# Kernel optimization log

Hardware: AMD Instinct MI355X
Metric: run time of the kernel (lower is better)

The kernel has to match this reference:

```python
import jax, jax.numpy as jnp
import numpy as np

EMBED = 1024
HIDDEN = 4 * EMBED
NUM_EXPERTS = 8
TOP_K = 2


def setup_inputs() -> dict:
    key = jax.random.key(0)
    k_in, k_w1, k_b1, k_w2, k_b2 = jax.random.split(key, 5)
    s1 = 1.0 / np.sqrt(EMBED)
    s2 = 1.0 / np.sqrt(HIDDEN)
    return {
        "inputs": jax.random.normal(k_in, (8, 4096, EMBED), dtype=jnp.float32),
        "w1": jax.random.uniform(k_w1, (EMBED, HIDDEN), jnp.float32, -s1, s1),
        "b1": jax.random.uniform(k_b1, (HIDDEN,), jnp.float32, -s1, s1),
        "w2": jax.random.uniform(k_w2, (HIDDEN, NUM_EXPERTS), jnp.float32, -s2, s2),
        "b2": jax.random.uniform(k_b2, (NUM_EXPERTS,), jnp.float32, -s2, s2),
    }


def reference(inputs, w1, b1, w2, b2):
    # MLP scorer: [B,S,E] -> [B,S,H] -> [B,S,num_experts]
    h = jax.nn.relu(jnp.einsum("bse,eh->bsh", inputs, w1) + b1)
    score = jnp.einsum("bsh,hn->bsn", h, w2) + b2
    # top-k over expert dim
    _, topk_idx = jax.lax.top_k(score, TOP_K)  # [B,S,K]
    # scatter mask: True at top-k positions
    mask = jax.nn.one_hot(topk_idx, NUM_EXPERTS, dtype=jnp.bool_).any(axis=-2)  # [B,S,N]
    masked = jnp.where(mask, score, -jnp.inf)
    router_output = jax.nn.softmax(masked, axis=-1)
    return router_output, topk_idx
```

## Files before the change

### kernel.cpp

```cpp
#include <hip/hip_runtime.h>

#define T_TOK 32768
#define EDIM  1024
#define HDIM  4096
#define NEXP  8
#define TAU   1.0e-3f
#define MAXR  8192


typedef _Float16 f16x8 __attribute__((ext_vector_type(8)));
typedef _Float16 f16x4 __attribute__((ext_vector_type(4)));
typedef __attribute__((ext_vector_type(4))) float f32x4;
#define MFMA16(a, b, c) __builtin_amdgcn_mfma_f32_16x16x32_f16(a, b, c, 0, 0, 0)

__device__ __forceinline__ void gload16(const void* g, void* l) {
    __builtin_amdgcn_global_load_lds(
        (const __attribute__((address_space(1))) void*)g,
        (__attribute__((address_space(3))) void*)l, 16, 0, 0);
}

__global__ __launch_bounds__(256) void split_x_kernel(
    const float* __restrict__ x, _Float16* __restrict__ hi, int n4)
{
    int i = blockIdx.x * 256 + threadIdx.x;
    int stride = gridDim.x * 256;
    for (; i < n4; i += stride) {
        float4 v = ((const float4*)x)[i];
        f16x4 h;
        h[0] = (_Float16)v.x; h[1] = (_Float16)v.y;
        h[2] = (_Float16)v.z; h[3] = (_Float16)v.w;
        *(f16x4*)&hi[i * 4] = h;
    }
}

__global__ __launch_bounds__(256) void split_w1t_kernel(
    const float* __restrict__ w1, _Float16* __restrict__ thi)
{
    __shared__ float t[64][65];
    const int ht = blockIdx.x;
    const int et = blockIdx.y;
    const int tid = threadIdx.x;
    const int er = tid >> 6, hc = tid & 63;
#pragma unroll
    for (int rr = 0; rr < 16; ++rr) {
        int e = rr * 4 + er;
        t[e][hc] = w1[(size_t)(et * 64 + e) * HDIM + ht * 64 + hc];
    }
    __syncthreads();
    const int hl = tid >> 2, eg = tid & 3;
    size_t base = (size_t)(ht * 64 + hl) * EDIM + et * 64 + eg * 16;
#pragma unroll
    for (int q = 0; q < 4; ++q) {
        f16x4 a;
#pragma unroll
        for (int z = 0; z < 4; ++z) a[z] = (_Float16)t[eg * 16 + q * 4 + z][hl];
        *(f16x4*)&thi[base + q * 4] = a;
    }
}

__global__ __launch_bounds__(256, 3) void mfma_score_kernel(
    const _Float16* __restrict__ xhi, const _Float16* __restrict__ whi,
    const float* __restrict__ b1, const float* __restrict__ w2,
    float* __restrict__ part)
{
    __shared__ __align__(16) _Float16 A3[3 * 4096];
    __shared__ __align__(16) _Float16 B3[3 * 4096];

    const int bid = blockIdx.x;
    const int lg  = (bid & 7) * 1024 + (bid >> 3);
    const int ht  = (lg >> 10) * 4 + (lg & 3);
    const int mt  = (lg & 1023) >> 2;
    const int m0 = mt * 128;
    const int h0 = ht * 128;
    const int tid = threadIdx.x;
    const int l = tid & 63;
    const int wid = tid >> 6;
    const int wm = wid >> 1, wn = wid & 1;

    const int srow = tid >> 2;
    const int sg = (tid & 3) ^ ((srow >> 1) & 3);
    const size_t xa0 = (size_t)(m0 + srow) * EDIM + sg * 8;
    const size_t xa1 = (size_t)(m0 + 64 + srow) * EDIM + sg * 8;
    const size_t wa0 = (size_t)(h0 + srow) * EDIM + sg * 8;
    const size_t wa1 = (size_t)(h0 + 64 + srow) * EDIM + sg * 8;
    const int ldst = tid * 16;

    const int lrow = l & 15, lslot = l >> 4;
    const int rslot = lslot ^ ((lrow >> 1) & 3);
    const int aoff = (wm * 64 + lrow) * 64 + rslot * 16;
    const int boff = (wn * 64 + lrow) * 64 + rslot * 16;

    f32x4 accA[4][4];
    const f32x4 zz = {0.f, 0.f, 0.f, 0.f};
#pragma unroll
    for (int i = 0; i < 4; ++i)
#pragma unroll
        for (int j = 0; j < 4; ++j) accA[i][j] = zz;

    auto stage = [&](int s, int bb) {
        const int k0 = s * 32;
        gload16(xhi + xa0 + k0, (char*)A3 + bb * 8192 + ldst);
        gload16(xhi + xa1 + k0, (char*)A3 + bb * 8192 + 4096 + ldst);
        gload16(whi + wa0 + k0, (char*)B3 + bb * 8192 + ldst);
        gload16(whi + wa1 + k0, (char*)B3 + bb * 8192 + 4096 + ldst);
    };
    auto compute = [&](int bb) {
        const char* Ab = (const char*)A3 + bb * 8192;
        const char* Bb = (const char*)B3 + bb * 8192;
        f16x8 ah[4];
#pragma unroll
        for (int mf = 0; mf < 4; ++mf)
            ah[mf] = *(const f16x8*)(Ab + aoff + mf * 1024);
        __builtin_amdgcn_s_setprio(1);
#pragma unroll
        for (int nf = 0; nf < 4; ++nf) {
            f16x8 bh = *(const f16x8*)(Bb + boff + nf * 1024);
#pragma unroll
            for (int mf = 0; mf < 4; ++mf)
                accA[mf][nf] = MFMA16(ah[mf], bh, accA[mf][nf]);
        }
        __builtin_amdgcn_s_setprio(0);
    };

#define WAITV4 do { asm volatile("s_waitcnt vmcnt(4)" ::: "memory"); \
                    __builtin_amdgcn_sched_barrier(0); } while (0)
#define WAITV0 do { asm volatile("s_waitcnt vmcnt(0)" ::: "memory"); \
                    __builtin_amdgcn_sched_barrier(0); } while (0)
#define BARR   do { __builtin_amdgcn_s_barrier(); \
                    __builtin_amdgcn_sched_barrier(0); } while (0)

    stage(0, 0);
    stage(1, 1);

    for (int t = 0; t < 30; t += 3) {
        WAITV4; BARR; stage(t + 2, (t + 2) % 3); compute(0);
        WAITV4; BARR; stage(t + 3, (t + 3) % 3); compute(1);
        WAITV4; BARR; stage(t + 4, (t + 4) % 3); compute(2);
    }
    WAITV4; BARR; compute(0);
    WAITV0; BARR; compute(1);

#undef WAITV4
#undef WAITV0
#undef BARR

    float b1r[4], w2r[4][8];
#pragma unroll
    for (int nf = 0; nf < 4; ++nf) {
        int h = h0 + wn * 64 + nf * 16 + lrow;
        b1r[nf] = b1[h];
#pragma unroll
        for (int n = 0; n < 8; ++n) w2r[nf][n] = w2[(size_t)h * NEXP + n];
    }

    const int b0 = l & 1, b1b = (l >> 1) & 1, b2 = (l >> 2) & 1, b3 = (l >> 3) & 1;
    const int regf = (b0 << 1) | b1b;
    const int n0e  = b2 * 4 + b3 * 2;
    float outq[4][2];

#pragma unroll
    for (int q = 0; q < 4; ++q) {
        float v[32];
#pragma unroll
        for (int i = 0; i < 32; ++i) v[i] = 0.f;
#pragma unroll
        for (int reg = 0; reg < 4; ++reg)
#pragma unroll
            for (int nf = 0; nf < 4; ++nf) {
                float hv = fmaxf(accA[q][nf][reg] + b1r[nf], 0.f);
#pragma unroll
                for (int n = 0; n < 8; ++n)
                    v[reg * 8 + n] = fmaf(hv, w2r[nf][n], v[reg * 8 + n]);
            }
        float t1[16];
#pragma unroll
        for (int i = 0; i < 16; ++i) {
            float keep = b0 ? v[i + 16] : v[i];
            float send = b0 ? v[i] : v[i + 16];
            t1[i] = keep + __shfl_xor(send, 1);
        }
        float t2[8];
#pragma unroll
        for (int i = 0; i < 8; ++i) {
            float keep = b1b ? t1[i + 8] : t1[i];
            float send = b1b ? t1[i] : t1[i + 8];
            t2[i] = keep + __shfl_xor(send, 2);
        }
        float t3[4];
#pragma unroll
        for (int i = 0; i < 4; ++i) {
            float keep = b2 ? t2[i + 4] : t2[i];
            float send = b2 ? t2[i] : t2[i + 4];
            t3[i] = keep + __shfl_xor(send, 4);
        }
#pragma unroll
        for (int j = 0; j < 2; ++j) {
            float keep = b3 ? t3[j + 2] : t3[j];
            float send = b3 ? t3[j] : t3[j + 2];
            outq[q][j] = keep + __shfl_xor(send, 8);
        }
    }

    __syncthreads();
    float* red = (float*)A3;
    if (wn == 1) {
#pragma unroll
        for (int q = 0; q < 4; ++q) {
            red[(wm * 64 + l) * 8 + q * 2 + 0] = outq[q][0];
            red[(wm * 64 + l) * 8 + q * 2 + 1] = outq[q][1];
        }
    }
    __syncthreads();
    if (wn == 0) {
#pragma unroll
        for (int q = 0; q < 4; ++q) {
            float a = outq[q][0] + red[(wm * 64 + l) * 8 + q * 2 + 0];
            float b = outq[q][1] + red[(wm * 64 + l) * 8 + q * 2 + 1];
            int rl = wm * 64 + q * 16 + lslot * 4 + regf;
            *(float2*)&part[((size_t)ht * T_TOK + m0 + rl) * NEXP + n0e] =
                make_float2(a, b);
        }
    }
}

__global__ void zero_counter_kernel(int* c) {
    if (threadIdx.x == 0 && blockIdx.x == 0) *c = 0;
}

__global__ __launch_bounds__(256) void router_finish_kernel(
    const float* __restrict__ part, const float* __restrict__ b2,
    float* __restrict__ out, int nparts, int* __restrict__ counter,
    int* __restrict__ list)
{
    int t = blockIdx.x * 256 + threadIdx.x;
    if (t >= T_TOK) return;

    float s[NEXP];
#pragma unroll
    for (int n = 0; n < NEXP; ++n) s[n] = 0.f;
    for (int p = 0; p < nparts; ++p) {
        const float* ps = part + (size_t)p * T_TOK * NEXP + (size_t)t * NEXP;
        float4 v0 = *reinterpret_cast<const float4*>(ps);
        float4 v1 = *reinterpret_cast<const float4*>(ps + 4);
        s[0] += v0.x; s[1] += v0.y; s[2] += v0.z; s[3] += v0.w;
        s[4] += v1.x; s[5] += v1.y; s[6] += v1.z; s[7] += v1.w;
    }
#pragma unroll
    for (int n = 0; n < NEXP; ++n) s[n] += b2[n];

    int i1 = 0; float v1 = s[0];
#pragma unroll
    for (int n = 1; n < NEXP; ++n) { if (s[n] > v1) { v1 = s[n]; i1 = n; } }
    int i2 = -1; float v2 = -3.402823466e38f;
#pragma unroll
    for (int n = 0; n < NEXP; ++n) { if (n != i1 && s[n] > v2) { v2 = s[n]; i2 = n; } }
    float v3 = -3.402823466e38f;
#pragma unroll
    for (int n = 0; n < NEXP; ++n) { if (n != i1 && n != i2 && s[n] > v3) v3 = s[n]; }

    if ((v1 - v2) < TAU || (v2 - v3) < TAU) {
        int pos = atomicAdd(counter, 1);
        list[pos] = t;
    }

    float e2 = expf(v2 - v1);
    float denom = 1.f + e2;
    float p1 = 1.f / denom;
    float p2 = e2 / denom;
#pragma unroll
    for (int n = 0; n < NEXP; ++n)
        out[(size_t)t * NEXP + n] = (n == i1) ? p1 : ((n == i2) ? p2 : 0.f);
    out[(size_t)T_TOK * NEXP + (size_t)t * 2 + 0] = (float)i1;
    out[(size_t)T_TOK * NEXP + (size_t)t * 2 + 1] = (float)i2;
}

__global__ __launch_bounds__(256) void gather_x_kernel(
    const float* __restrict__ x, const int* __restrict__ counter,
    const int* __restrict__ list, float* __restrict__ xg)
{
    int cnt = *counter; if (cnt > MAXR) cnt = MAXR;
    for (int g = blockIdx.x; g < cnt; g += gridDim.x) {
        const int t = list[g];
        float4 v = ((const float4*)(x + (size_t)t * EDIM))[threadIdx.x];
        ((float4*)(xg + (size_t)g * EDIM))[threadIdx.x] = v;
    }
}

__global__ __launch_bounds__(256) void refine_gemm_kernel(
    const float* __restrict__ xg, const float* __restrict__ w1,
    const float* __restrict__ b1, const float* __restrict__ w2,
    const int* __restrict__ counter, float* __restrict__ rpart)
{
    int cnt = *counter; if (cnt > MAXR) cnt = MAXR;
    const int m0 = blockIdx.y * 64;
    if (m0 >= cnt) return;
    const int ht = blockIdx.x;
    const int h0 = ht * 128;
    const int tid = threadIdx.x;
    const int tx = tid & 15, ty = tid >> 4;

    __shared__ float xs[16][68];
    __shared__ float wsh[16][128];

    float acc[4][8];
#pragma unroll
    for (int i = 0; i < 4; ++i)
#pragma unroll
        for (int j = 0; j < 8; ++j) acc[i][j] = 0.f;

    const int lk = tid & 15, lt = tid >> 4;
    const int lh = tid & 127, lkg = tid >> 7;

    for (int k0 = 0; k0 < EDIM; k0 += 16) {
        __syncthreads();
#pragma unroll
        for (int r = 0; r < 4; ++r)
            xs[lk][lt + r * 16] = xg[(size_t)(m0 + lt + r * 16) * EDIM + k0 + lk];
#pragma unroll
        for (int r = 0; r < 8; ++r)
            wsh[lkg + r * 2][lh] = w1[(size_t)(k0 + lkg + r * 2) * HDIM + h0 + lh];
        __syncthreads();
#pragma unroll
        for (int k = 0; k < 16; ++k) {
            float a[4], b[8];
#pragma unroll
            for (int i = 0; i < 4; ++i) a[i] = xs[k][ty * 4 + i];
            *reinterpret_cast<float4*>(&b[0]) = *reinterpret_cast<const float4*>(&wsh[k][tx * 8]);
            *reinterpret_cast<float4*>(&b[4]) = *reinterpret_cast<const float4*>(&wsh[k][tx * 8 + 4]);
#pragma unroll
            for (int i = 0; i < 4; ++i)
#pragma unroll
                for (int j = 0; j < 8; ++j)
                    acc[i][j] = fmaf(a[i], b[j], acc[i][j]);
        }
    }

    float sred[4][NEXP];
#pragma unroll
    for (int i = 0; i < 4; ++i) {
        float hv[8];
#pragma unroll
        for (int j = 0; j < 8; ++j)
            hv[j] = fmaxf(acc[i][j] + b1[h0 + tx * 8 + j], 0.f);
#pragma unroll
        for (int n = 0; n < NEXP; ++n) {
            float ssum = 0.f;
#pragma unroll
            for (int j = 0; j < 8; ++j)
                ssum = fmaf(hv[j], w2[(size_t)(h0 + tx * 8 + j) * NEXP + n], ssum);
            sred[i][n] = ssum;
        }
    }
#pragma unroll
    for (int i = 0; i < 4; ++i)
#pragma unroll
        for (int n = 0; n < NEXP; ++n) {
            float v = sred[i][n];
            v += __shfl_xor(v, 1);
            v += __shfl_xor(v, 2);
            v += __shfl_xor(v, 4);
            v += __shfl_xor(v, 8);
            sred[i][n] = v;
        }

    if (tx == 0) {
#pragma unroll
        for (int i = 0; i < 4; ++i) {
            int g = m0 + ty * 4 + i;
            if (g < cnt) {
#pragma unroll
                for (int n = 0; n < NEXP; ++n)
                    rpart[((size_t)g * 32 + ht) * NEXP + n] = sred[i][n];
            }
        }
    }
}

__global__ __launch_bounds__(256) void refine_final_kernel(
    const int* __restrict__ counter, const int* __restrict__ list,
    const float* __restrict__ rpart, const float* __restrict__ b2,
    float* __restrict__ out)
{
    int cnt = *counter; if (cnt > MAXR) cnt = MAXR;
    const int g = blockIdx.x * 256 + threadIdx.x;
    if (g >= cnt) return;
    const int t = list[g];
    float s[NEXP];
#pragma unroll
    for (int n = 0; n < NEXP; ++n) s[n] = b2[n];
    for (int r = 0; r < 32; ++r)
#pragma unroll
        for (int n = 0; n < NEXP; ++n)
            s[n] += rpart[((size_t)g * 32 + r) * NEXP + n];

    int i1 = 0; float v1 = s[0];
#pragma unroll
    for (int n = 1; n < NEXP; ++n) { if (s[n] > v1) { v1 = s[n]; i1 = n; } }
    int i2 = -1; float v2 = -3.402823466e38f;
#pragma unroll
    for (int n = 0; n < NEXP; ++n) { if (n != i1 && s[n] > v2) { v2 = s[n]; i2 = n; } }

    float e2 = expf(v2 - v1);
    float denom = 1.f + e2;
    float p1 = 1.f / denom;
    float p2 = e2 / denom;
#pragma unroll
    for (int n = 0; n < NEXP; ++n)
        out[(size_t)t * NEXP + n] = (n == i1) ? p1 : ((n == i2) ? p2 : 0.f);
    out[(size_t)T_TOK * NEXP + (size_t)t * 2 + 0] = (float)i1;
    out[(size_t)T_TOK * NEXP + (size_t)t * 2 + 1] = (float)i2;
}

#define BM 128
#define BH 128
#define BK 16
#define NHT (HDIM / BH)

__global__ __launch_bounds__(256) void score_gemm_kernel(
    const float* __restrict__ x, const float* __restrict__ w1,
    const float* __restrict__ b1, const float* __restrict__ w2,
    float* __restrict__ dst)
{
    __shared__ float xs[BK][BM + 4];
    __shared__ float wsh[BK][BH];
    __shared__ float w2s[BH * NEXP];
    __shared__ float b1s[BH];

    const int htile = blockIdx.x;
    const int mtile = blockIdx.y;
    const int h0 = htile * BH;
    const int m0 = mtile * BM;
    const int tid = threadIdx.x;
    const int tx = tid & 15;
    const int ty = tid >> 4;

    {
        float4 v = *reinterpret_cast<const float4*>(&w2[(size_t)h0 * NEXP + tid * 4]);
        *reinterpret_cast<float4*>(&w2s[tid * 4]) = v;
        if (tid < BH) b1s[tid] = b1[h0 + tid];
    }

    float acc[8][8];
#pragma unroll
    for (int i = 0; i < 8; ++i)
#pragma unroll
        for (int j = 0; j < 8; ++j) acc[i][j] = 0.f;

    const int e_off = tid & 15;
    const int t_row = tid >> 4;
    const int h_off = tid & 127;
    const int k_off = tid >> 7;

    for (int k0 = 0; k0 < EDIM; k0 += BK) {
        __syncthreads();
#pragma unroll
        for (int r = 0; r < 8; ++r) {
            int tok = t_row + r * 16;
            xs[e_off][tok] = x[(size_t)(m0 + tok) * EDIM + k0 + e_off];
        }
#pragma unroll
        for (int r = 0; r < 8; ++r) {
            int k = k_off + r * 2;
            wsh[k][h_off] = w1[(size_t)(k0 + k) * HDIM + h0 + h_off];
        }
        __syncthreads();
#pragma unroll
        for (int k = 0; k < BK; ++k) {
            float a[8], b[8];
            *reinterpret_cast<float4*>(&a[0]) = *reinterpret_cast<const float4*>(&xs[k][ty * 8]);
            *reinterpret_cast<float4*>(&a[4]) = *reinterpret_cast<const float4*>(&xs[k][ty * 8 + 4]);
            *reinterpret_cast<float4*>(&b[0]) = *reinterpret_cast<const float4*>(&wsh[k][tx * 8]);
            *reinterpret_cast<float4*>(&b[4]) = *reinterpret_cast<const float4*>(&wsh[k][tx * 8 + 4]);
#pragma unroll
            for (int i = 0; i < 8; ++i)
#pragma unroll
                for (int j = 0; j < 8; ++j)
                    acc[i][j] = fmaf(a[i], b[j], acc[i][j]);
        }
    }

    float sred[8][NEXP];
#pragma unroll
    for (int i = 0; i < 8; ++i) {
        float hv[8];
#pragma unroll
        for (int j = 0; j < 8; ++j)
            hv[j] = fmaxf(acc[i][j] + b1s[tx * 8 + j], 0.f);
#pragma unroll
        for (int n = 0; n < NEXP; ++n) {
            float ssum = 0.f;
#pragma unroll
            for (int j = 0; j < 8; ++j)
                ssum = fmaf(hv[j], w2s[(tx * 8 + j) * NEXP + n], ssum);
            sred[i][n] = ssum;
        }
    }
#pragma unroll
    for (int i = 0; i < 8; ++i)
#pragma unroll
        for (int n = 0; n < NEXP; ++n) {
            float v = sred[i][n];
            v += __shfl_xor(v, 1);
            v += __shfl_xor(v, 2);
            v += __shfl_xor(v, 4);
            v += __shfl_xor(v, 8);
            sred[i][n] = v;
        }

    if (tx == 0) {
        float* slice = dst + (size_t)htile * T_TOK * NEXP;
#pragma unroll
        for (int i = 0; i < 8; ++i)
#pragma unroll
            for (int n = 0; n < NEXP; ++n)
                slice[(size_t)(m0 + ty * 8 + i) * NEXP + n] = sred[i][n];
    }
}

__global__ __launch_bounds__(256) void finish_simple_kernel(
    const float* __restrict__ part, const float* __restrict__ b2,
    float* __restrict__ out, int nparts)
{
    int t = blockIdx.x * 256 + threadIdx.x;
    if (t >= T_TOK) return;
    float s[NEXP];
#pragma unroll
    for (int n = 0; n < NEXP; ++n) s[n] = 0.f;
    for (int p = 0; p < nparts; ++p) {
        const float* ps = part + (size_t)p * T_TOK * NEXP + (size_t)t * NEXP;
        float4 v0 = *reinterpret_cast<const float4*>(ps);
        float4 v1 = *reinterpret_cast<const float4*>(ps + 4);
        s[0] += v0.x; s[1] += v0.y; s[2] += v0.z; s[3] += v0.w;
        s[4] += v1.x; s[5] += v1.y; s[6] += v1.z; s[7] += v1.w;
    }
#pragma unroll
    for (int n = 0; n < NEXP; ++n) s[n] += b2[n];
    int i1 = 0; float v1 = s[0];
#pragma unroll
    for (int n = 1; n < NEXP; ++n) { if (s[n] > v1) { v1 = s[n]; i1 = n; } }
    int i2 = -1; float v2 = -3.402823466e38f;
#pragma unroll
    for (int n = 0; n < NEXP; ++n) { if (n != i1 && s[n] > v2) { v2 = s[n]; i2 = n; } }
    float e2 = expf(v2 - v1);
    float denom = 1.f + e2;
    float p1 = 1.f / denom;
    float p2 = e2 / denom;
#pragma unroll
    for (int n = 0; n < NEXP; ++n)
        out[(size_t)t * NEXP + n] = (n == i1) ? p1 : ((n == i2) ? p2 : 0.f);
    out[(size_t)T_TOK * NEXP + (size_t)t * 2 + 0] = (float)i1;
    out[(size_t)T_TOK * NEXP + (size_t)t * 2 + 1] = (float)i2;
}

extern "C" void kernel_launch(void* const* d_in, const int* in_sizes, int n_in,
                              void* d_out, int out_size, void* d_ws, size_t ws_size,
                              hipStream_t stream)
{
    const float* x  = (const float*)d_in[0];
    const float* w1 = (const float*)d_in[1];
    const float* b1 = (const float*)d_in[2];
    const float* w2 = (const float*)d_in[3];
    const float* b2 = (const float*)d_in[4];
    float* out = (float*)d_out;

    char* ws = (char*)d_ws;
    _Float16* xhi = (_Float16*)ws;
    _Float16* whi = (_Float16*)(ws + 67108864);
    float* part   = (float*)(ws + 75497472);
    int* counter  = (int*)(ws + 109051904);
    int* list     = (int*)(ws + 109052928);
    float* xg     = (float*)(ws + 109184000);
    float* rpart  = (float*)(ws + 142738432);
    const size_t NEED = 151127040;

    if (ws_size >= NEED) {
        split_x_kernel<<<2048, 256, 0, stream>>>(x, xhi, (T_TOK * EDIM) / 4);
        dim3 tg(64, 16);
        split_w1t_kernel<<<tg, 256, 0, stream>>>(w1, whi);
        mfma_score_kernel<<<8192, 256, 0, stream>>>(xhi, whi, b1, w2, part);
        zero_counter_kernel<<<1, 64, 0, stream>>>(counter);
        router_finish_kernel<<<T_TOK / 256, 256, 0, stream>>>(part, b2, out, 32,
                                                              counter, list);
        gather_x_kernel<<<256, 256, 0, stream>>>(x, counter, list, xg);
        dim3 rg(32, MAXR / 64);
        refine_gemm_kernel<<<rg, 256, 0, stream>>>(xg, w1, b1, w2, counter, rpart);
        refine_final_kernel<<<MAXR / 256, 256, 0, stream>>>(counter, list, rpart,
                                                            b2, out);
    } else {
        float* p1 = (float*)d_ws;
        dim3 grid(NHT, T_TOK / BM);
        score_gemm_kernel<<<grid, 256, 0, stream>>>(x, w1, b1, w2, p1);
        finish_simple_kernel<<<T_TOK / 256, 256, 0, stream>>>(p1, b2, out, NHT);
    }
}
```

Before: 609.2 us.

## Enlarge MFMA score tile to 256x128 tokens per block

Doubles the token dimension of each block tile in the fp16 MFMA scoring GEMM from 128 to 256 rows, so each wave accumulates 8x4 MFMA fragments, and halves the grid to 4096 blocks. Each W1 tile loaded into LDS is now reused across twice as many tokens, which cuts global/LDS traffic per FLOP. In exchange the accumulator register count doubles and LDS per block grows, so occupancy drops from 3 to 2 blocks per CU. The pipeline wait count, epilogue reduction layout and output indexing are adjusted to match.

```diff
diff --git a/kernel.cpp b/kernel.cpp
--- a/kernel.cpp
+++ b/kernel.cpp
@@ -58,19 +58,19 @@
     }
 }
 
-__global__ __launch_bounds__(256, 3) void mfma_score_kernel(
+__global__ __launch_bounds__(256, 2) void mfma_score_kernel(
     const _Float16* __restrict__ xhi, const _Float16* __restrict__ whi,
     const float* __restrict__ b1, const float* __restrict__ w2,
     float* __restrict__ part)
 {
-    __shared__ __align__(16) _Float16 A3[3 * 4096];
+    __shared__ __align__(16) _Float16 A3[3 * 8192];
     __shared__ __align__(16) _Float16 B3[3 * 4096];
 
     const int bid = blockIdx.x;
-    const int lg  = (bid & 7) * 1024 + (bid >> 3);
-    const int ht  = (lg >> 10) * 4 + (lg & 3);
-    const int mt  = (lg & 1023) >> 2;
-    const int m0 = mt * 128;
+    const int lg  = (bid & 7) * 512 + (bid >> 3);
+    const int ht  = (lg >> 9) * 4 + (lg & 3);
+    const int mt  = (lg & 511) >> 2;
+    const int m0 = mt * 256;
     const int h0 = ht * 128;
     const int tid = threadIdx.x;
     const int l = tid & 63;
@@ -79,50 +79,52 @@
 
     const int srow = tid >> 2;
     const int sg = (tid & 3) ^ ((srow >> 1) & 3);
-    const size_t xa0 = (size_t)(m0 + srow) * EDIM + sg * 8;
-    const size_t xa1 = (size_t)(m0 + 64 + srow) * EDIM + sg * 8;
-    const size_t wa0 = (size_t)(h0 + srow) * EDIM + sg * 8;
-    const size_t wa1 = (size_t)(h0 + 64 + srow) * EDIM + sg * 8;
     const int ldst = tid * 16;
 
     const int lrow = l & 15, lslot = l >> 4;
     const int rslot = lslot ^ ((lrow >> 1) & 3);
-    const int aoff = (wm * 64 + lrow) * 64 + rslot * 16;
+    const int aoff = (wm * 128 + lrow) * 64 + rslot * 16;
     const int boff = (wn * 64 + lrow) * 64 + rslot * 16;
 
-    f32x4 accA[4][4];
+    f32x4 acc[8][4];
     const f32x4 zz = {0.f, 0.f, 0.f, 0.f};
 #pragma unroll
-    for (int i = 0; i < 4; ++i)
-#pragma unroll
-        for (int j = 0; j < 4; ++j) accA[i][j] = zz;
+    for (int i = 0; i < 8; ++i)
+#pragma unroll
+        for (int j = 0; j < 4; ++j) acc[i][j] = zz;
 
     auto stage = [&](int s, int bb) {
         const int k0 = s * 32;
-        gload16(xhi + xa0 + k0, (char*)A3 + bb * 8192 + ldst);
-        gload16(xhi + xa1 + k0, (char*)A3 + bb * 8192 + 4096 + ldst);
-        gload16(whi + wa0 + k0, (char*)B3 + bb * 8192 + ldst);
-        gload16(whi + wa1 + k0, (char*)B3 + bb * 8192 + 4096 + ldst);
+        char* Ab = (char*)A3 + bb * 16384;
+        char* Bb = (char*)B3 + bb * 8192;
+#pragma unroll
+        for (int r = 0; r < 4; ++r)
+            gload16(xhi + (size_t)(m0 + r * 64 + srow) * EDIM + sg * 8 + k0,
+                    Ab + r * 4096 + ldst);
+#pragma unroll
+        for (int r = 0; r < 2; ++r)
+            gload16(whi + (size_t)(h0 + r * 64 + srow) * EDIM + sg * 8 + k0,
+                    Bb + r * 4096 + ldst);
     };
     auto compute = [&](int bb) {
-        const char* Ab = (const char*)A3 + bb * 8192;
+        const char* Ab = (const char*)A3 + bb * 16384;
         const char* Bb = (const char*)B3 + bb * 8192;
-        f16x8 ah[4];
-#pragma unroll
-        for (int mf = 0; mf < 4; ++mf)
+        f16x8 ah[8];
+#pragma unroll
+        for (int mf = 0; mf < 8; ++mf)
             ah[mf] = *(const f16x8*)(Ab + aoff + mf * 1024);
         __builtin_amdgcn_s_setprio(1);
 #pragma unroll
         for (int nf = 0; nf < 4; ++nf) {
             f16x8 bh = *(const f16x8*)(Bb + boff + nf * 1024);
 #pragma unroll
-            for (int mf = 0; mf < 4; ++mf)
-                accA[mf][nf] = MFMA16(ah[mf], bh, accA[mf][nf]);
+            for (int mf = 0; mf < 8; ++mf)
+                acc[mf][nf] = MFMA16(ah[mf], bh, acc[mf][nf]);
         }
         __builtin_amdgcn_s_setprio(0);
     };
 
-#define WAITV4 do { asm volatile("s_waitcnt vmcnt(4)" ::: "memory"); \
+#define WAITV6 do { asm volatile("s_waitcnt vmcnt(6)" ::: "memory"); \
                     __builtin_amdgcn_sched_barrier(0); } while (0)
 #define WAITV0 do { asm volatile("s_waitcnt vmcnt(0)" ::: "memory"); \
                     __builtin_amdgcn_sched_barrier(0); } while (0)
@@ -133,14 +135,14 @@
     stage(1, 1);
 
     for (int t = 0; t < 30; t += 3) {
-        WAITV4; BARR; stage(t + 2, (t + 2) % 3); compute(0);
-        WAITV4; BARR; stage(t + 3, (t + 3) % 3); compute(1);
-        WAITV4; BARR; stage(t + 4, (t + 4) % 3); compute(2);
-    }
-    WAITV4; BARR; compute(0);
+        WAITV6; BARR; stage(t + 2, (t + 2) % 3); compute(0);
+        WAITV6; BARR; stage(t + 3, (t + 3) % 3); compute(1);
+        WAITV6; BARR; stage(t + 4, (t + 4) % 3); compute(2);
+    }
+    WAITV6; BARR; compute(0);
     WAITV0; BARR; compute(1);
 
-#undef WAITV4
+#undef WAITV6
 #undef WAITV0
 #undef BARR
 
@@ -156,10 +158,10 @@
     const int b0 = l & 1, b1b = (l >> 1) & 1, b2 = (l >> 2) & 1, b3 = (l >> 3) & 1;
     const int regf = (b0 << 1) | b1b;
     const int n0e  = b2 * 4 + b3 * 2;
-    float outq[4][2];
-
-#pragma unroll
-    for (int q = 0; q < 4; ++q) {
+    float outq[8][2];
+
+#pragma unroll
+    for (int q = 0; q < 8; ++q) {
         float v[32];
 #pragma unroll
         for (int i = 0; i < 32; ++i) v[i] = 0.f;
@@ -167,7 +169,7 @@
         for (int reg = 0; reg < 4; ++reg)
 #pragma unroll
             for (int nf = 0; nf < 4; ++nf) {
-                float hv = fmaxf(accA[q][nf][reg] + b1r[nf], 0.f);
+                float hv = fmaxf(acc[q][nf][reg] + b1r[nf], 0.f);
 #pragma unroll
                 for (int n = 0; n < 8; ++n)
                     v[reg * 8 + n] = fmaf(hv, w2r[nf][n], v[reg * 8 + n]);
@@ -205,18 +207,18 @@
     float* red = (float*)A3;
     if (wn == 1) {
 #pragma unroll
-        for (int q = 0; q < 4; ++q) {
-            red[(wm * 64 + l) * 8 + q * 2 + 0] = outq[q][0];
-            red[(wm * 64 + l) * 8 + q * 2 + 1] = outq[q][1];
+        for (int q = 0; q < 8; ++q) {
+            red[(wm * 64 + l) * 16 + q * 2 + 0] = outq[q][0];
+            red[(wm * 64 + l) * 16 + q * 2 + 1] = outq[q][1];
         }
     }
     __syncthreads();
     if (wn == 0) {
 #pragma unroll
-        for (int q = 0; q < 4; ++q) {
-            float a = outq[q][0] + red[(wm * 64 + l) * 8 + q * 2 + 0];
-            float b = outq[q][1] + red[(wm * 64 + l) * 8 + q * 2 + 1];
-            int rl = wm * 64 + q * 16 + lslot * 4 + regf;
+        for (int q = 0; q < 8; ++q) {
+            float a = outq[q][0] + red[(wm * 64 + l) * 16 + q * 2 + 0];
+            float b = outq[q][1] + red[(wm * 64 + l) * 16 + q * 2 + 1];
+            int rl = wm * 128 + q * 16 + lslot * 4 + regf;
             *(float2*)&part[((size_t)ht * T_TOK + m0 + rl) * NEXP + n0e] =
                 make_float2(a, b);
         }
@@ -577,7 +579,7 @@
         split_x_kernel<<<2048, 256, 0, stream>>>(x, xhi, (T_TOK * EDIM) / 4);
         dim3 tg(64, 16);
         split_w1t_kernel<<<tg, 256, 0, stream>>>(w1, whi);
-        mfma_score_kernel<<<8192, 256, 0, stream>>>(xhi, whi, b1, w2, part);
+        mfma_score_kernel<<<4096, 256, 0, stream>>>(xhi, whi, b1, w2, part);
         zero_counter_kernel<<<1, 64, 0, stream>>>(counter);
         router_finish_kernel<<<T_TOK / 256, 256, 0, stream>>>(part, b2, out, 32,
                                                               counter, list);
```

After: 700.0 us. +14.9%, slower.

## Switch score GEMM to double-buffered LDS, raise occupancy, fold counter zeroing

Applied to the files above, without the earlier changes.

The score GEMM's LDS pipeline drops from triple to double buffering, which frees shared memory, and launch bounds are raised from 3 to 4 blocks per CU. The block-to-tile mapping is changed so consecutive blocks walk all 32 hidden tiles of one row tile before moving on. The separate zero-counter kernel is removed and its work is folded into the W1 transpose kernel, saving one launch. Waiting for all loads (vmcnt 0) each step lowers prefetch depth, which may expose global-load latency that the higher occupancy is meant to hide.

```diff
diff --git a/kernel.cpp b/kernel.cpp
--- a/kernel.cpp
+++ b/kernel.cpp
@@ -34,12 +34,14 @@
 }
 
 __global__ __launch_bounds__(256) void split_w1t_kernel(
-    const float* __restrict__ w1, _Float16* __restrict__ thi)
+    const float* __restrict__ w1, _Float16* __restrict__ thi,
+    int* __restrict__ counter)
 {
     __shared__ float t[64][65];
     const int ht = blockIdx.x;
     const int et = blockIdx.y;
     const int tid = threadIdx.x;
+    if (ht == 0 && et == 0 && tid == 0) *counter = 0;
     const int er = tid >> 6, hc = tid & 63;
 #pragma unroll
     for (int rr = 0; rr < 16; ++rr) {
@@ -58,18 +60,18 @@
     }
 }
 
-__global__ __launch_bounds__(256, 3) void mfma_score_kernel(
+__global__ __launch_bounds__(256, 4) void mfma_score_kernel(
     const _Float16* __restrict__ xhi, const _Float16* __restrict__ whi,
     const float* __restrict__ b1, const float* __restrict__ w2,
     float* __restrict__ part)
 {
-    __shared__ __align__(16) _Float16 A3[3 * 4096];
-    __shared__ __align__(16) _Float16 B3[3 * 4096];
+    __shared__ __align__(16) _Float16 A2[2 * 4096];
+    __shared__ __align__(16) _Float16 B2[2 * 4096];
 
     const int bid = blockIdx.x;
     const int lg  = (bid & 7) * 1024 + (bid >> 3);
-    const int ht  = (lg >> 10) * 4 + (lg & 3);
-    const int mt  = (lg & 1023) >> 2;
+    const int ht  = lg & 31;
+    const int mt  = lg >> 5;
     const int m0 = mt * 128;
     const int h0 = ht * 128;
     const int tid = threadIdx.x;
@@ -90,23 +92,23 @@
     const int aoff = (wm * 64 + lrow) * 64 + rslot * 16;
     const int boff = (wn * 64 + lrow) * 64 + rslot * 16;
 
-    f32x4 accA[4][4];
+    f32x4 acc[4][4];
     const f32x4 zz = {0.f, 0.f, 0.f, 0.f};
 #pragma unroll
     for (int i = 0; i < 4; ++i)
 #pragma unroll
-        for (int j = 0; j < 4; ++j) accA[i][j] = zz;
+        for (int j = 0; j < 4; ++j) acc[i][j] = zz;
 
     auto stage = [&](int s, int bb) {
         const int k0 = s * 32;
-        gload16(xhi + xa0 + k0, (char*)A3 + bb * 8192 + ldst);
-        gload16(xhi + xa1 + k0, (char*)A3 + bb * 8192 + 4096 + ldst);
-        gload16(whi + wa0 + k0, (char*)B3 + bb * 8192 + ldst);
-        gload16(whi + wa1 + k0, (char*)B3 + bb * 8192 + 4096 + ldst);
+        gload16(xhi + xa0 + k0, (char*)A2 + bb * 8192 + ldst);
+        gload16(xhi + xa1 + k0, (char*)A2 + bb * 8192 + 4096 + ldst);
+        gload16(whi + wa0 + k0, (char*)B2 + bb * 8192 + ldst);
+        gload16(whi + wa1 + k0, (char*)B2 + bb * 8192 + 4096 + ldst);
     };
     auto compute = [&](int bb) {
-        const char* Ab = (const char*)A3 + bb * 8192;
-        const char* Bb = (const char*)B3 + bb * 8192;
+        const char* Ab = (const char*)A2 + bb * 8192;
+        const char* Bb = (const char*)B2 + bb * 8192;
         f16x8 ah[4];
 #pragma unroll
         for (int mf = 0; mf < 4; ++mf)
@@ -117,30 +119,26 @@
             f16x8 bh = *(const f16x8*)(Bb + boff + nf * 1024);
 #pragma unroll
             for (int mf = 0; mf < 4; ++mf)
-                accA[mf][nf] = MFMA16(ah[mf], bh, accA[mf][nf]);
+                acc[mf][nf] = MFMA16(ah[mf], bh, acc[mf][nf]);
         }
         __builtin_amdgcn_s_setprio(0);
     };
 
-#define WAITV4 do { asm volatile("s_waitcnt vmcnt(4)" ::: "memory"); \
-                    __builtin_amdgcn_sched_barrier(0); } while (0)
 #define WAITV0 do { asm volatile("s_waitcnt vmcnt(0)" ::: "memory"); \
                     __builtin_amdgcn_sched_barrier(0); } while (0)
 #define BARR   do { __builtin_amdgcn_s_barrier(); \
                     __builtin_amdgcn_sched_barrier(0); } while (0)
 
     stage(0, 0);
-    stage(1, 1);
-
-    for (int t = 0; t < 30; t += 3) {
-        WAITV4; BARR; stage(t + 2, (t + 2) % 3); compute(0);
-        WAITV4; BARR; stage(t + 3, (t + 3) % 3); compute(1);
-        WAITV4; BARR; stage(t + 4, (t + 4) % 3); compute(2);
-    }
-    WAITV4; BARR; compute(0);
-    WAITV0; BARR; compute(1);
-
-#undef WAITV4
+    for (int t = 0; t < 32; t += 2) {
+        WAITV0; BARR;
+        if (t + 1 < 32) stage(t + 1, 1);
+        compute(0);
+        WAITV0; BARR;
+        if (t + 2 < 32) stage(t + 2, 0);
+        compute(1);
+    }
+
 #undef WAITV0
 #undef BARR
 
@@ -167,7 +165,7 @@
         for (int reg = 0; reg < 4; ++reg)
 #pragma unroll
             for (int nf = 0; nf < 4; ++nf) {
-                float hv = fmaxf(accA[q][nf][reg] + b1r[nf], 0.f);
+                float hv = fmaxf(acc[q][nf][reg] + b1r[nf], 0.f);
 #pragma unroll
                 for (int n = 0; n < 8; ++n)
                     v[reg * 8 + n] = fmaf(hv, w2r[nf][n], v[reg * 8 + n]);
@@ -202,7 +200,7 @@
     }
 
     __syncthreads();
-    float* red = (float*)A3;
+    float* red = (float*)A2;
     if (wn == 1) {
 #pragma unroll
         for (int q = 0; q < 4; ++q) {
@@ -221,10 +219,6 @@
                 make_float2(a, b);
         }
     }
-}
-
-__global__ void zero_counter_kernel(int* c) {
-    if (threadIdx.x == 0 && blockIdx.x == 0) *c = 0;
 }
 
 __global__ __launch_bounds__(256) void router_finish_kernel(
@@ -576,9 +570,8 @@
     if (ws_size >= NEED) {
         split_x_kernel<<<2048, 256, 0, stream>>>(x, xhi, (T_TOK * EDIM) / 4);
         dim3 tg(64, 16);
-        split_w1t_kernel<<<tg, 256, 0, stream>>>(w1, whi);
+        split_w1t_kernel<<<tg, 256, 0, stream>>>(w1, whi, counter);
         mfma_score_kernel<<<8192, 256, 0, stream>>>(xhi, whi, b1, w2, part);
-        zero_counter_kernel<<<1, 64, 0, stream>>>(counter);
         router_finish_kernel<<<T_TOK / 256, 256, 0, stream>>>(part, b2, out, 32,
                                                               counter, list);
         gather_x_kernel<<<256, 256, 0, stream>>>(x, counter, list, xg);
```

Result: slower. 815.6 us (+33.9%).
